# Optimization experiments

Hardware: AMD Instinct MI355X
Metric: run time of the kernel (lower is better)

The kernel has to match this reference:

```python
import jax, jax.numpy as jnp
import numpy as np

EPS = 1e-8


def setup_inputs() -> dict:
    key = jax.random.key(0)
    k1, k2 = jax.random.split(key)
    a = jax.random.normal(k1, (1, 256, 128, 128), dtype=jnp.float32)
    b = jax.random.normal(k2, (1, 256, 128, 128), dtype=jnp.float32)
    return {"a": a, "b": b}


def reference(a, b):
    # a: [n, c, h, w] rendered feats; b: [n, c, h2, w2] style feats (n == 1)
    n, c, h, w = a.shape
    a_flat = a.reshape(n, c, -1)            # [n, c, hw]
    b_flat = b.reshape(n, c, -1)            # [n, c, h2w2]

    # argmin_cos_distance: channel-wise L2 normalize, cosine distance, argmin
    b_norm = jnp.sqrt((b_flat * b_flat).sum(1, keepdims=True) + EPS)
    b_n = b_flat / (b_norm + EPS)
    a_norm = jnp.sqrt((a_flat * a_flat).sum(1, keepdims=True) + EPS)
    a_n = a_flat / (a_norm + EPS)
    d_mat = 1.0 - jnp.einsum('ncp,ncq->npq', a_n, b_n)   # [n, hw, h2w2]
    z_best = jnp.argmin(d_mat, axis=2)                    # [n, hw]

    # nn_feat_replace: gather matched (unnormalized) style features
    idx = jnp.broadcast_to(z_best[:, None, :], b_flat.shape)
    target = jnp.take_along_axis(b_flat, idx, axis=2).reshape(n, c, h, w)

    # cos_loss(a, target): cosine distance over channel dim, mean over pixels
    an = jnp.sqrt((a * a).sum(1, keepdims=True))
    tn = jnp.sqrt((target * target).sum(1, keepdims=True))
    cossim = ((a / (an + EPS)) * (target / (tn + EPS))).sum(1)  # [n, h, w]
    return (1.0 - cossim).mean()
```

## Files before the change

kernel.cpp:

```cpp
#include <hip/hip_runtime.h>
#include <stdint.h>

#define EPS 1e-8f

constexpr int HW = 16384;
constexpr int BM = 128;
constexpr int NG = 2048;

typedef __attribute__((ext_vector_type(4))) float floatx4;
typedef __attribute__((ext_vector_type(4))) int   intx4;
typedef __attribute__((ext_vector_type(8))) int   intx8;
typedef unsigned char u8;
typedef unsigned int u32;
typedef unsigned long long u64;

typedef const __attribute__((address_space(1))) u32 gas_u32;
typedef __attribute__((address_space(3))) u32 las_u32;
__device__ inline void stage16(const void* g, void* l) {
    __builtin_amdgcn_global_load_lds((gas_u32*)g, (las_u32*)l, 16, 0, 0);
}

__device__ inline u32 pk4(float x0, float x1, float x2, float x3) {
    int t = __builtin_amdgcn_cvt_pk_fp8_f32(x0, x1, 0, false);
    t = __builtin_amdgcn_cvt_pk_fp8_f32(x2, x3, t, true);
    return (u32)t;
}

__device__ inline float getc(const float4& f, int j) {
    return (j == 0) ? f.x : (j == 1) ? f.y : (j == 2) ? f.z : f.w;
}

__global__ __launch_bounds__(512) void prep_kernel(const float* __restrict__ a,
                                                   const float* __restrict__ b,
                                                   float* __restrict__ sumsq_a,
                                                   float* __restrict__ sumsq_b,
                                                   u8* __restrict__ aF, u8* __restrict__ bF,
                                                   u64* __restrict__ packed,
                                                   float* __restrict__ out) {
    __shared__ float red[64][33];
    __shared__ float invb_sh[32];
    const int tid = threadIdx.x;
    const int pg = tid & 7, tc = tid >> 3;
    const int p0 = blockIdx.x * 32, pb = pg * 4;
    const int c0 = tc * 4;
    const u32 fb = (u32)((c0 >> 7) * 2048 + ((c0 >> 4) & 1) * 1024 + (c0 & 15));
    const u32 qr16 = (u32)(((c0 >> 5) & 3) * 16);

    if (blockIdx.x < 32) packed[(size_t)blockIdx.x * 512 + tid] = 0ull;
    if (blockIdx.x == 0 && tid == 0) *out = 0.f;

    float4 bv[4], av[4];
    #pragma unroll
    for (int i = 0; i < 4; ++i)
        bv[i] = *(const float4*)&b[(size_t)(c0 + i) * HW + p0 + pb];
    #pragma unroll
    for (int i = 0; i < 4; ++i)
        av[i] = *(const float4*)&a[(size_t)(c0 + i) * HW + p0 + pb];

    float s0 = 0.f, s1 = 0.f, s2 = 0.f, s3 = 0.f;
    #pragma unroll
    for (int i = 0; i < 4; ++i) {
        s0 += bv[i].x * bv[i].x; s1 += bv[i].y * bv[i].y;
        s2 += bv[i].z * bv[i].z; s3 += bv[i].w * bv[i].w;
    }
    red[tc][pb] = s0; red[tc][pb + 1] = s1; red[tc][pb + 2] = s2; red[tc][pb + 3] = s3;
    __syncthreads();
    if (tid < 32) {
        float B = 0.f;
        #pragma unroll
        for (int j = 0; j < 64; ++j) B += red[j][tid];
        sumsq_b[p0 + tid] = B;
        invb_sh[tid] = 1.0f / (sqrtf(B + EPS) + EPS);
    }
    __syncthreads();

    #pragma unroll
    for (int j = 0; j < 4; ++j) {
        const int p = p0 + pb + j;
        const float inv = invb_sh[pb + j];
        u32 wv = pk4(getc(bv[0], j) * inv, getc(bv[1], j) * inv,
                     getc(bv[2], j) * inv, getc(bv[3], j) * inv);
        *(u32*)(bF + ((size_t)(p >> 4) << 12) + fb + (qr16 + (u32)(p & 15)) * 16) = wv;
    }

    s0 = s1 = s2 = s3 = 0.f;
    #pragma unroll
    for (int i = 0; i < 4; ++i) {
        s0 += av[i].x * av[i].x; s1 += av[i].y * av[i].y;
        s2 += av[i].z * av[i].z; s3 += av[i].w * av[i].w;
    }
    red[tc][pb] = s0; red[tc][pb + 1] = s1; red[tc][pb + 2] = s2; red[tc][pb + 3] = s3;
    #pragma unroll
    for (int j = 0; j < 4; ++j) {
        const int p = p0 + pb + j;
        u32 wv = pk4(getc(av[0], j), getc(av[1], j), getc(av[2], j), getc(av[3], j));
        *(u32*)(aF + ((size_t)(p >> 4) << 12) + fb + (qr16 + (u32)(p & 15)) * 16) = wv;
    }
    __syncthreads();
    if (tid < 32) {
        float A = 0.f;
        #pragma unroll
        for (int j = 0; j < 64; ++j) A += red[j][tid];
        sumsq_a[p0 + tid] = A;
    }
}

__global__ __launch_bounds__(256, 3) void gemm_argmax(const u8* __restrict__ aF,
                                                      const u8* __restrict__ bF,
                                                      u64* __restrict__ packed) {
    __shared__ u8 sB[2][16384];
    const int tid = threadIdx.x;
    const int w = tid >> 6, lane = tid & 63;
    const int q4 = lane >> 4, r15 = lane & 15;
    const int wm = w >> 1, wn = w & 1;

    const u32 bid = blockIdx.x;
    const u32 ng = bid & 7;
    const u32 mt = bid >> 3;
    const int p0 = (int)mt * BM;

    const u8* gA = aF + (((size_t)(mt * 8 + wm * 4)) << 12) + (u32)lane * 16;
    intx8 Afr[4][2];
    #pragma unroll
    for (int mi = 0; mi < 4; ++mi)
        #pragma unroll
        for (int kb = 0; kb < 2; ++kb) {
            intx4 lo = *(const intx4*)(gA + (u32)(mi * 4096 + kb * 2048));
            intx4 hi = *(const intx4*)(gA + (u32)(mi * 4096 + kb * 2048 + 1024));
            Afr[mi][kb] = __builtin_shufflevector(lo, hi, 0, 1, 2, 3, 4, 5, 6, 7);
        }

    const u8* gQ = bF + ((size_t)ng << 19);
    const u32 so = (u32)w * 4096u + (u32)lane * 16u;

    #pragma unroll
    for (int i = 0; i < 4; ++i)
        stage16(gQ + so + (u32)(i * 1024), &sB[0][w * 4096 + i * 1024]);

    float bestv[4][4];
    u32   bestq[4][4];
    #pragma unroll
    for (int mi = 0; mi < 4; ++mi)
        #pragma unroll
        for (int r = 0; r < 4; ++r) { bestv[mi][r] = -3.4e38f; bestq[mi][r] = 0; }

    u32 q0 = ng * 2048 + wn * 32 + (u32)r15;
    const floatx4 C64 = {64.f, 64.f, 64.f, 64.f};
    const int SCL = 0x7F7F7F7F;

    __syncthreads();

    int x = 0;
    for (int qt = 0; qt < 32; ++qt) {
        if (qt < 31) {
            const u8* gs = gQ + (u32)(qt + 1) * 16384u + so;
            u8* ls = &sB[x ^ 1][w * 4096];
            #pragma unroll
            for (int i = 0; i < 4; ++i)
                stage16(gs + (u32)(i * 1024), ls + i * 1024);
        }

        const u8* Lb = &sB[x][(u32)(wn * 2) * 4096u + (u32)lane * 16u];
        floatx4 acc[4][2];
        intx8 B0, B1;

        { intx4 lo = *(const intx4*)(Lb);
          intx4 hi = *(const intx4*)(Lb + 1024);
          B0 = __builtin_shufflevector(lo, hi, 0, 1, 2, 3, 4, 5, 6, 7); }
        { intx4 lo = *(const intx4*)(Lb + 4096);
          intx4 hi = *(const intx4*)(Lb + 4096 + 1024);
          B1 = __builtin_shufflevector(lo, hi, 0, 1, 2, 3, 4, 5, 6, 7); }
        __builtin_amdgcn_s_setprio(1);
        #pragma unroll
        for (int mi = 0; mi < 4; ++mi)
            acc[mi][0] = __builtin_amdgcn_mfma_scale_f32_16x16x128_f8f6f4(
                Afr[mi][0], B0, C64, 0, 0, 0, SCL, 0, SCL);
        #pragma unroll
        for (int mi = 0; mi < 4; ++mi)
            acc[mi][1] = __builtin_amdgcn_mfma_scale_f32_16x16x128_f8f6f4(
                Afr[mi][0], B1, C64, 0, 0, 0, SCL, 0, SCL);
        __builtin_amdgcn_s_setprio(0);

        { intx4 lo = *(const intx4*)(Lb + 2048);
          intx4 hi = *(const intx4*)(Lb + 2048 + 1024);
          B0 = __builtin_shufflevector(lo, hi, 0, 1, 2, 3, 4, 5, 6, 7); }
        { intx4 lo = *(const intx4*)(Lb + 4096 + 2048);
          intx4 hi = *(const intx4*)(Lb + 4096 + 2048 + 1024);
          B1 = __builtin_shufflevector(lo, hi, 0, 1, 2, 3, 4, 5, 6, 7); }
        __builtin_amdgcn_s_setprio(1);
        #pragma unroll
        for (int mi = 0; mi < 4; ++mi)
            acc[mi][0] = __builtin_amdgcn_mfma_scale_f32_16x16x128_f8f6f4(
                Afr[mi][1], B0, acc[mi][0], 0, 0, 0, SCL, 0, SCL);
        #pragma unroll
        for (int mi = 0; mi < 4; ++mi)
            acc[mi][1] = __builtin_amdgcn_mfma_scale_f32_16x16x128_f8f6f4(
                Afr[mi][1], B1, acc[mi][1], 0, 0, 0, SCL, 0, SCL);
        __builtin_amdgcn_s_setprio(0);

        #pragma unroll
        for (int mi = 0; mi < 4; ++mi)
            #pragma unroll
            for (int r = 0; r < 4; ++r) {
                float v = acc[mi][0][r];
                bool gt = v > bestv[mi][r];
                bestv[mi][r] = gt ? v : bestv[mi][r];
                bestq[mi][r] = gt ? q0 : bestq[mi][r];
            }
        #pragma unroll
        for (int mi = 0; mi < 4; ++mi)
            #pragma unroll
            for (int r = 0; r < 4; ++r) {
                float v = acc[mi][1][r];
                bool gt = v > bestv[mi][r];
                bestv[mi][r] = gt ? v : bestv[mi][r];
                bestq[mi][r] = gt ? (q0 + 16u) : bestq[mi][r];
            }
        q0 += 64u;

        __syncthreads();
        x ^= 1;
    }

    #pragma unroll
    for (int mi = 0; mi < 4; ++mi)
        #pragma unroll
        for (int r = 0; r < 4; ++r) {
            u64 pk = ((u64)__float_as_uint(bestv[mi][r]) << 32)
                   | (u64)(0xFFFFFFFFu - bestq[mi][r]);
            #pragma unroll
            for (int d = 1; d < 16; d <<= 1) {
                u64 o = __shfl_xor((unsigned long long)pk, d);
                pk = o > pk ? o : pk;
            }
            if (r15 == 0)
                atomicMax(&packed[p0 + wm * 64 + mi * 16 + q4 * 4 + r], pk);
        }
}

__global__ void loss_kernel(const u64* __restrict__ packed,
                            const float* __restrict__ sumsq_a, const float* __restrict__ sumsq_b,
                            float* __restrict__ out) {
    int p = blockIdx.x * 256 + threadIdx.x;
    u64 pk = packed[p];
    float s = __uint_as_float((u32)(pk >> 32)) - 64.0f;
    u32 q = 0xFFFFFFFFu - (u32)(pk & 0xFFFFFFFFull);
    float A = sumsq_a[p], B = sumsq_b[q];
    float dot = s * (sqrtf(B + EPS) + EPS);
    float cossim = dot / ((sqrtf(A) + EPS) * (sqrtf(B) + EPS));
    float v = (1.0f - cossim) * (1.0f / (float)HW);
    #pragma unroll
    for (int d = 1; d < 64; d <<= 1) v += __shfl_xor(v, d);
    if ((threadIdx.x & 63) == 0) atomicAdd(out, v);
}

extern "C" void kernel_launch(void* const* d_in, const int* in_sizes, int n_in,
                              void* d_out, int out_size, void* d_ws, size_t ws_size,
                              hipStream_t stream) {
    const float* a = (const float*)d_in[0];
    const float* b = (const float*)d_in[1];
    float* out = (float*)d_out;
    char* ws = (char*)d_ws;

    u8*    aF      = (u8*)ws;
    u8*    bF      = (u8*)(ws + (size_t)4 * 1024 * 1024);
    float* sumsq_a = (float*)(ws + (size_t)8 * 1024 * 1024);
    float* sumsq_b = sumsq_a + HW;
    u64*   packed  = (u64*)(sumsq_b + HW);

    prep_kernel<<<dim3(HW / 32), 512, 0, stream>>>(a, b, sumsq_a, sumsq_b, aF, bF, packed, out);
    gemm_argmax<<<dim3((HW / BM) * (HW / NG)), 256, 0, stream>>>(aF, bF, packed);
    loss_kernel<<<dim3(HW / 256), 256, 0, stream>>>(packed, sumsq_a, sumsq_b, out);
}
```

Before: 145.3 us.

## Double workgroup to 8 waves and software-pipeline MFMA with deferred argmax

```diff
diff --git a/kernel.cpp b/kernel.cpp
--- a/kernel.cpp
+++ b/kernel.cpp
@@ -105,7 +105,58 @@
     }
 }
 
-__global__ __launch_bounds__(256, 3) void gemm_argmax(const u8* __restrict__ aF,
+#define MFMA1(A_, B_, C_) __builtin_amdgcn_mfma_scale_f32_16x16x128_f8f6f4( \
+        (A_), (B_), (C_), 0, 0, 0, SCL, 0, SCL)
+
+#define LDB(off_) __builtin_shufflevector(                                  \
+        *(const intx4*)(Lb + (off_)), *(const intx4*)(Lb + (off_) + 1024),  \
+        0, 1, 2, 3, 4, 5, 6, 7)
+
+#define MFMA_QT(acc_, buf_) do {                                            \
+    const u8* Lb = &sB[buf_][(u32)(wn * 2) * 4096u + (u32)lane * 16u];      \
+    intx8 Bk0n0 = LDB(0);                                                   \
+    intx8 Bk0n1 = LDB(4096);                                                \
+    __builtin_amdgcn_s_setprio(1);                                          \
+    acc_[0][0] = MFMA1(Afr[0][0], Bk0n0, C64);                              \
+    acc_[1][0] = MFMA1(Afr[1][0], Bk0n0, C64);                              \
+    acc_[0][1] = MFMA1(Afr[0][0], Bk0n1, C64);                              \
+    acc_[1][1] = MFMA1(Afr[1][0], Bk0n1, C64);                              \
+    __builtin_amdgcn_s_setprio(0);                                          \
+    intx8 Bk1n0 = LDB(2048);                                                \
+    intx8 Bk1n1 = LDB(4096 + 2048);                                         \
+    __builtin_amdgcn_s_setprio(1);                                          \
+    acc_[0][0] = MFMA1(Afr[0][1], Bk1n0, acc_[0][0]);                       \
+    acc_[1][0] = MFMA1(Afr[1][1], Bk1n0, acc_[1][0]);                       \
+    acc_[0][1] = MFMA1(Afr[0][1], Bk1n1, acc_[0][1]);                       \
+    acc_[1][1] = MFMA1(Afr[1][1], Bk1n1, acc_[1][1]);                       \
+    __builtin_amdgcn_s_setprio(0);                                          \
+} while (0)
+
+#define ARGMAX_QT(acc_, qt_) do {                                           \
+    const u32 qb_ = q0 + (u32)(qt_) * 64u;                                  \
+    _Pragma("unroll")                                                       \
+    for (int mi = 0; mi < 2; ++mi) {                                        \
+        _Pragma("unroll")                                                   \
+        for (int ni = 0; ni < 2; ++ni) {                                    \
+            const u32 qc_ = qb_ + (u32)(ni * 16);                           \
+            _Pragma("unroll")                                               \
+            for (int r = 0; r < 4; ++r) {                                   \
+                float v_ = acc_[mi][ni][r];                                 \
+                bool gt_ = v_ > bestv[mi][r];                               \
+                bestv[mi][r] = gt_ ? v_ : bestv[mi][r];                     \
+                bestq[mi][r] = gt_ ? qc_ : bestq[mi][r];                    \
+            }                                                               \
+        }                                                                   \
+    }                                                                       \
+} while (0)
+
+#define STAGE(buf_, qt_) do {                                               \
+    const u8* gs_ = gQ + (u32)(qt_) * 16384u + so;                          \
+    stage16(gs_, &sB[buf_][wso]);                                           \
+    stage16(gs_ + 1024, &sB[buf_][wso + 1024]);                             \
+} while (0)
+
+__global__ __launch_bounds__(512, 4) void gemm_argmax(const u8* __restrict__ aF,
                                                       const u8* __restrict__ bF,
                                                       u64* __restrict__ packed) {
     __shared__ u8 sB[2][16384];
@@ -119,111 +170,70 @@
     const u32 mt = bid >> 3;
     const int p0 = (int)mt * BM;
 
-    const u8* gA = aF + (((size_t)(mt * 8 + wm * 4)) << 12) + (u32)lane * 16;
-    intx8 Afr[4][2];
-    #pragma unroll
-    for (int mi = 0; mi < 4; ++mi)
-        #pragma unroll
-        for (int kb = 0; kb < 2; ++kb) {
-            intx4 lo = *(const intx4*)(gA + (u32)(mi * 4096 + kb * 2048));
-            intx4 hi = *(const intx4*)(gA + (u32)(mi * 4096 + kb * 2048 + 1024));
-            Afr[mi][kb] = __builtin_shufflevector(lo, hi, 0, 1, 2, 3, 4, 5, 6, 7);
-        }
+    const u8* gA = aF + (((size_t)(mt * 8 + wm * 2)) << 12) + (u32)lane * 16;
+    intx8 Afr[2][2];
+    #pragma unroll
+    for (int mi = 0; mi < 2; ++mi)
+        #pragma unroll
+        for (int kb = 0; kb < 2; ++kb)
+            Afr[mi][kb] = __builtin_shufflevector(
+                *(const intx4*)(gA + (u32)(mi * 4096 + kb * 2048)),
+                *(const intx4*)(gA + (u32)(mi * 4096 + kb * 2048 + 1024)),
+                0, 1, 2, 3, 4, 5, 6, 7);
 
     const u8* gQ = bF + ((size_t)ng << 19);
-    const u32 so = (u32)w * 4096u + (u32)lane * 16u;
-
-    #pragma unroll
-    for (int i = 0; i < 4; ++i)
-        stage16(gQ + so + (u32)(i * 1024), &sB[0][w * 4096 + i * 1024]);
-
-    float bestv[4][4];
-    u32   bestq[4][4];
-    #pragma unroll
-    for (int mi = 0; mi < 4; ++mi)
+    const u32 so  = (u32)w * 2048u + (u32)lane * 16u;
+    const u32 wso = (u32)w * 2048u;
+
+    float bestv[2][4];
+    u32   bestq[2][4];
+    #pragma unroll
+    for (int mi = 0; mi < 2; ++mi)
         #pragma unroll
         for (int r = 0; r < 4; ++r) { bestv[mi][r] = -3.4e38f; bestq[mi][r] = 0; }
 
-    u32 q0 = ng * 2048 + wn * 32 + (u32)r15;
+    const u32 q0 = ng * 2048 + wn * 32 + (u32)r15;
     const floatx4 C64 = {64.f, 64.f, 64.f, 64.f};
     const int SCL = 0x7F7F7F7F;
 
-    __syncthreads();
-
-    int x = 0;
-    for (int qt = 0; qt < 32; ++qt) {
-        if (qt < 31) {
-            const u8* gs = gQ + (u32)(qt + 1) * 16384u + so;
-            u8* ls = &sB[x ^ 1][w * 4096];
-            #pragma unroll
-            for (int i = 0; i < 4; ++i)
-                stage16(gs + (u32)(i * 1024), ls + i * 1024);
-        }
-
-        const u8* Lb = &sB[x][(u32)(wn * 2) * 4096u + (u32)lane * 16u];
-        floatx4 acc[4][2];
-        intx8 B0, B1;
-
-        { intx4 lo = *(const intx4*)(Lb);
-          intx4 hi = *(const intx4*)(Lb + 1024);
-          B0 = __builtin_shufflevector(lo, hi, 0, 1, 2, 3, 4, 5, 6, 7); }
-        { intx4 lo = *(const intx4*)(Lb + 4096);
-          intx4 hi = *(const intx4*)(Lb + 4096 + 1024);
-          B1 = __builtin_shufflevector(lo, hi, 0, 1, 2, 3, 4, 5, 6, 7); }
-        __builtin_amdgcn_s_setprio(1);
-        #pragma unroll
-        for (int mi = 0; mi < 4; ++mi)
-            acc[mi][0] = __builtin_amdgcn_mfma_scale_f32_16x16x128_f8f6f4(
-                Afr[mi][0], B0, C64, 0, 0, 0, SCL, 0, SCL);
-        #pragma unroll
-        for (int mi = 0; mi < 4; ++mi)
-            acc[mi][1] = __builtin_amdgcn_mfma_scale_f32_16x16x128_f8f6f4(
-                Afr[mi][0], B1, C64, 0, 0, 0, SCL, 0, SCL);
-        __builtin_amdgcn_s_setprio(0);
-
-        { intx4 lo = *(const intx4*)(Lb + 2048);
-          intx4 hi = *(const intx4*)(Lb + 2048 + 1024);
-          B0 = __builtin_shufflevector(lo, hi, 0, 1, 2, 3, 4, 5, 6, 7); }
-        { intx4 lo = *(const intx4*)(Lb + 4096 + 2048);
-          intx4 hi = *(const intx4*)(Lb + 4096 + 2048 + 1024);
-          B1 = __builtin_shufflevector(lo, hi, 0, 1, 2, 3, 4, 5, 6, 7); }
-        __builtin_amdgcn_s_setprio(1);
-        #pragma unroll
-        for (int mi = 0; mi < 4; ++mi)
-            acc[mi][0] = __builtin_amdgcn_mfma_scale_f32_16x16x128_f8f6f4(
-                Afr[mi][1], B0, acc[mi][0], 0, 0, 0, SCL, 0, SCL);
-        #pragma unroll
-        for (int mi = 0; mi < 4; ++mi)
-            acc[mi][1] = __builtin_amdgcn_mfma_scale_f32_16x16x128_f8f6f4(
-                Afr[mi][1], B1, acc[mi][1], 0, 0, 0, SCL, 0, SCL);
-        __builtin_amdgcn_s_setprio(0);
-
-        #pragma unroll
-        for (int mi = 0; mi < 4; ++mi)
-            #pragma unroll
-            for (int r = 0; r < 4; ++r) {
-                float v = acc[mi][0][r];
-                bool gt = v > bestv[mi][r];
-                bestv[mi][r] = gt ? v : bestv[mi][r];
-                bestq[mi][r] = gt ? q0 : bestq[mi][r];
-            }
-        #pragma unroll
-        for (int mi = 0; mi < 4; ++mi)
-            #pragma unroll
-            for (int r = 0; r < 4; ++r) {
-                float v = acc[mi][1][r];
-                bool gt = v > bestv[mi][r];
-                bestv[mi][r] = gt ? v : bestv[mi][r];
-                bestq[mi][r] = gt ? (q0 + 16u) : bestq[mi][r];
-            }
-        q0 += 64u;
-
+    floatx4 accA[2][2], accB[2][2];
+
+    STAGE(0, 0);
+    __syncthreads();
+
+    STAGE(1, 1);
+    MFMA_QT(accA, 0);
+    __syncthreads();
+
+    STAGE(0, 2);
+    MFMA_QT(accB, 1);
+    ARGMAX_QT(accA, 0);
+    __syncthreads();
+
+    for (int i = 1; i <= 14; ++i) {
+        const int qtA = 2 * i;
+        STAGE(1, qtA + 1);
+        MFMA_QT(accA, 0);
+        ARGMAX_QT(accB, qtA - 1);
         __syncthreads();
-        x ^= 1;
-    }
-
-    #pragma unroll
-    for (int mi = 0; mi < 4; ++mi)
+
+        STAGE(0, qtA + 2);
+        MFMA_QT(accB, 1);
+        ARGMAX_QT(accA, qtA);
+        __syncthreads();
+    }
+
+    STAGE(1, 31);
+    MFMA_QT(accA, 0);
+    ARGMAX_QT(accB, 29);
+    __syncthreads();
+
+    MFMA_QT(accB, 1);
+    ARGMAX_QT(accA, 30);
+    ARGMAX_QT(accB, 31);
+
+    #pragma unroll
+    for (int mi = 0; mi < 2; ++mi)
         #pragma unroll
         for (int r = 0; r < 4; ++r) {
             u64 pk = ((u64)__float_as_uint(bestv[mi][r]) << 32)
@@ -234,7 +244,7 @@
                 pk = o > pk ? o : pk;
             }
             if (r15 == 0)
-                atomicMax(&packed[p0 + wm * 64 + mi * 16 + q4 * 4 + r], pk);
+                atomicMax(&packed[p0 + wm * 32 + mi * 16 + q4 * 4 + r], pk);
         }
 }
 
@@ -269,6 +279,6 @@
     u64*   packed  = (u64*)(sumsq_b + HW);
 
     prep_kernel<<<dim3(HW / 32), 512, 0, stream>>>(a, b, sumsq_a, sumsq_b, aF, bF, packed, out);
-    gemm_argmax<<<dim3((HW / BM) * (HW / NG)), 256, 0, stream>>>(aF, bF, packed);
+    gemm_argmax<<<dim3((HW / BM) * (HW / NG)), 512, 0, stream>>>(aF, bF, packed);
     loss_kernel<<<dim3(HW / 256), 256, 0, stream>>>(packed, sumsq_a, sumsq_b, out);
 }
```

New measurement: 165.7 us. 14.0% more time.

## Split prep into partial sum-of-squares pass and normalize/pack pass

Applied to the files above, without the earlier changes.

```diff
diff --git a/kernel.cpp b/kernel.cpp
--- a/kernel.cpp
+++ b/kernel.cpp
@@ -30,24 +30,63 @@
     return (j == 0) ? f.x : (j == 1) ? f.y : (j == 2) ? f.z : f.w;
 }
 
-__global__ __launch_bounds__(512) void prep_kernel(const float* __restrict__ a,
-                                                   const float* __restrict__ b,
-                                                   float* __restrict__ sumsq_a,
-                                                   float* __restrict__ sumsq_b,
-                                                   u8* __restrict__ aF, u8* __restrict__ bF,
-                                                   u64* __restrict__ packed,
-                                                   float* __restrict__ out) {
-    __shared__ float red[64][33];
-    __shared__ float invb_sh[32];
+__global__ __launch_bounds__(256) void prep1_kernel(const float* __restrict__ a,
+                                                    const float* __restrict__ b,
+                                                    float* __restrict__ apart,
+                                                    float* __restrict__ bpart,
+                                                    u64* __restrict__ packed,
+                                                    float* __restrict__ out) {
     const int tid = threadIdx.x;
-    const int pg = tid & 7, tc = tid >> 3;
-    const int p0 = blockIdx.x * 32, pb = pg * 4;
+    const u32 bid = blockIdx.x;
+    const int pg = (int)(bid >> 4), cg = (int)(bid & 15);
+    const int p = pg * 256 + tid;
+    const int c0 = cg * 16;
+
+    if (bid < 64) packed[(size_t)bid * 256 + tid] = 0ull;
+    if (bid == 0 && tid == 0) *out = 0.f;
+
+    float sb = 0.f, sa = 0.f;
+    #pragma unroll
+    for (int i = 0; i < 16; ++i) {
+        float xb = b[(size_t)(c0 + i) * HW + p];
+        sb += xb * xb;
+    }
+    #pragma unroll
+    for (int i = 0; i < 16; ++i) {
+        float xa = a[(size_t)(c0 + i) * HW + p];
+        sa += xa * xa;
+    }
+    bpart[(size_t)cg * HW + p] = sb;
+    apart[(size_t)cg * HW + p] = sa;
+}
+
+__global__ __launch_bounds__(256) void prep2_kernel(const float* __restrict__ a,
+                                                    const float* __restrict__ b,
+                                                    const float* __restrict__ apart,
+                                                    const float* __restrict__ bpart,
+                                                    float* __restrict__ sumsq_a,
+                                                    float* __restrict__ sumsq_b,
+                                                    u8* __restrict__ aF, u8* __restrict__ bF) {
+    __shared__ float invb_sh[16];
+    const int tid = threadIdx.x;
+    const int pg = tid & 3, tc = tid >> 2;
+    const int p0 = blockIdx.x * 16, pb = pg * 4;
     const int c0 = tc * 4;
     const u32 fb = (u32)((c0 >> 7) * 2048 + ((c0 >> 4) & 1) * 1024 + (c0 & 15));
     const u32 qr16 = (u32)(((c0 >> 5) & 3) * 16);
 
-    if (blockIdx.x < 32) packed[(size_t)blockIdx.x * 512 + tid] = 0ull;
-    if (blockIdx.x == 0 && tid == 0) *out = 0.f;
+    if (tid < 16) {
+        const int p = p0 + tid;
+        float B = 0.f, A = 0.f;
+        #pragma unroll
+        for (int j = 0; j < 16; ++j) {
+            B += bpart[(size_t)j * HW + p];
+            A += apart[(size_t)j * HW + p];
+        }
+        sumsq_b[p] = B;
+        sumsq_a[p] = A;
+        invb_sh[tid] = 1.0f / (sqrtf(B + EPS) + EPS);
+    }
 
     float4 bv[4], av[4];
     #pragma unroll
@@ -56,22 +95,6 @@
     #pragma unroll
     for (int i = 0; i < 4; ++i)
         av[i] = *(const float4*)&a[(size_t)(c0 + i) * HW + p0 + pb];
-
-    float s0 = 0.f, s1 = 0.f, s2 = 0.f, s3 = 0.f;
-    #pragma unroll
-    for (int i = 0; i < 4; ++i) {
-        s0 += bv[i].x * bv[i].x; s1 += bv[i].y * bv[i].y;
-        s2 += bv[i].z * bv[i].z; s3 += bv[i].w * bv[i].w;
-    }
-    red[tc][pb] = s0; red[tc][pb + 1] = s1; red[tc][pb + 2] = s2; red[tc][pb + 3] = s3;
-    __syncthreads();
-    if (tid < 32) {
-        float B = 0.f;
-        #pragma unroll
-        for (int j = 0; j < 64; ++j) B += red[j][tid];
-        sumsq_b[p0 + tid] = B;
-        invb_sh[tid] = 1.0f / (sqrtf(B + EPS) + EPS);
-    }
     __syncthreads();
 
     #pragma unroll
@@ -82,26 +105,11 @@
                      getc(bv[2], j) * inv, getc(bv[3], j) * inv);
         *(u32*)(bF + ((size_t)(p >> 4) << 12) + fb + (qr16 + (u32)(p & 15)) * 16) = wv;
     }
-
-    s0 = s1 = s2 = s3 = 0.f;
-    #pragma unroll
-    for (int i = 0; i < 4; ++i) {
-        s0 += av[i].x * av[i].x; s1 += av[i].y * av[i].y;
-        s2 += av[i].z * av[i].z; s3 += av[i].w * av[i].w;
-    }
-    red[tc][pb] = s0; red[tc][pb + 1] = s1; red[tc][pb + 2] = s2; red[tc][pb + 3] = s3;
     #pragma unroll
     for (int j = 0; j < 4; ++j) {
         const int p = p0 + pb + j;
         u32 wv = pk4(getc(av[0], j), getc(av[1], j), getc(av[2], j), getc(av[3], j));
         *(u32*)(aF + ((size_t)(p >> 4) << 12) + fb + (qr16 + (u32)(p & 15)) * 16) = wv;
-    }
-    __syncthreads();
-    if (tid < 32) {
-        float A = 0.f;
-        #pragma unroll
-        for (int j = 0; j < 64; ++j) A += red[j][tid];
-        sumsq_a[p0 + tid] = A;
     }
 }
 
@@ -124,11 +132,11 @@
     #pragma unroll
     for (int mi = 0; mi < 4; ++mi)
         #pragma unroll
-        for (int kb = 0; kb < 2; ++kb) {
-            intx4 lo = *(const intx4*)(gA + (u32)(mi * 4096 + kb * 2048));
-            intx4 hi = *(const intx4*)(gA + (u32)(mi * 4096 + kb * 2048 + 1024));
-            Afr[mi][kb] = __builtin_shufflevector(lo, hi, 0, 1, 2, 3, 4, 5, 6, 7);
-        }
+        for (int kb = 0; kb < 2; ++kb)
+            Afr[mi][kb] = __builtin_shufflevector(
+                *(const intx4*)(gA + (u32)(mi * 4096 + kb * 2048)),
+                *(const intx4*)(gA + (u32)(mi * 4096 + kb * 2048 + 1024)),
+                0, 1, 2, 3, 4, 5, 6, 7);
 
     const u8* gQ = bF + ((size_t)ng << 19);
     const u32 so = (u32)w * 4096u + (u32)lane * 16u;
@@ -267,8 +275,12 @@
     float* sumsq_a = (float*)(ws + (size_t)8 * 1024 * 1024);
     float* sumsq_b = sumsq_a + HW;
     u64*   packed  = (u64*)(sumsq_b + HW);
-
-    prep_kernel<<<dim3(HW / 32), 512, 0, stream>>>(a, b, sumsq_a, sumsq_b, aF, bF, packed, out);
+    float* apart   = (float*)(ws + (size_t)8 * 1024 * 1024 + 256 * 1024);
+    float* bpart   = apart + 16 * HW;
+
+    prep1_kernel<<<dim3(1024), 256, 0, stream>>>(a, b, apart, bpart, packed, out);
+    prep2_kernel<<<dim3(HW / 16), 256, 0, stream>>>(a, b, apart, bpart,
+                                                    sumsq_a, sumsq_b, aF, bF);
     gemm_argmax<<<dim3((HW / BM) * (HW / NG)), 256, 0, stream>>>(aF, bF, packed);
     loss_kernel<<<dim3(HW / 256), 256, 0, stream>>>(packed, sumsq_a, sumsq_b, out);
 }
```

New measurement: 154.7 us. 1.06x slower.

## Move b normalization from prep into GEMM epilogue, simplify prep kernel

Applied to the files above, without the earlier changes.

```diff
diff --git a/kernel.cpp b/kernel.cpp
--- a/kernel.cpp
+++ b/kernel.cpp
@@ -26,89 +26,59 @@
     return (u32)t;
 }
 
-__device__ inline float getc(const float4& f, int j) {
-    return (j == 0) ? f.x : (j == 1) ? f.y : (j == 2) ? f.z : f.w;
-}
-
-__global__ __launch_bounds__(512) void prep_kernel(const float* __restrict__ a,
+__global__ __launch_bounds__(256) void prep_kernel(const float* __restrict__ a,
                                                    const float* __restrict__ b,
                                                    float* __restrict__ sumsq_a,
                                                    float* __restrict__ sumsq_b,
                                                    u8* __restrict__ aF, u8* __restrict__ bF,
                                                    u64* __restrict__ packed,
                                                    float* __restrict__ out) {
-    __shared__ float red[64][33];
-    __shared__ float invb_sh[32];
+    __shared__ float redb[8][33];
+    __shared__ float reda[8][33];
     const int tid = threadIdx.x;
-    const int pg = tid & 7, tc = tid >> 3;
-    const int p0 = blockIdx.x * 32, pb = pg * 4;
-    const int c0 = tc * 4;
-    const u32 fb = (u32)((c0 >> 7) * 2048 + ((c0 >> 4) & 1) * 1024 + (c0 & 15));
-    const u32 qr16 = (u32)(((c0 >> 5) & 3) * 16);
-
-    if (blockIdx.x < 32) packed[(size_t)blockIdx.x * 512 + tid] = 0ull;
+    const int px = tid & 31, wg = tid >> 5;
+    const int p0 = blockIdx.x * 32;
+    const int p = p0 + px;
+    const int c0 = wg * 32;
+
+    if (blockIdx.x < 64) packed[(size_t)blockIdx.x * 256 + tid] = 0ull;
     if (blockIdx.x == 0 && tid == 0) *out = 0.f;
 
-    float4 bv[4], av[4];
-    #pragma unroll
-    for (int i = 0; i < 4; ++i)
-        bv[i] = *(const float4*)&b[(size_t)(c0 + i) * HW + p0 + pb];
-    #pragma unroll
-    for (int i = 0; i < 4; ++i)
-        av[i] = *(const float4*)&a[(size_t)(c0 + i) * HW + p0 + pb];
-
-    float s0 = 0.f, s1 = 0.f, s2 = 0.f, s3 = 0.f;
-    #pragma unroll
-    for (int i = 0; i < 4; ++i) {
-        s0 += bv[i].x * bv[i].x; s1 += bv[i].y * bv[i].y;
-        s2 += bv[i].z * bv[i].z; s3 += bv[i].w * bv[i].w;
-    }
-    red[tc][pb] = s0; red[tc][pb + 1] = s1; red[tc][pb + 2] = s2; red[tc][pb + 3] = s3;
+    const u32 slab = ((u32)(p >> 4)) << 12;
+    const u32 r16 = (u32)(p & 15) * 16;
+
+    float sb = 0.f, sa = 0.f;
+    #pragma unroll
+    for (int k = 0; k < 8; ++k) {
+        const int c = c0 + k * 4;
+        const u32 fo = (u32)((c >> 7) * 2048 + ((c >> 4) & 1) * 1024 + (c & 15))
+                     + (u32)(((c >> 5) & 3) * 256) + r16;
+        float x0 = b[(size_t)(c + 0) * HW + p], x1 = b[(size_t)(c + 1) * HW + p];
+        float x2 = b[(size_t)(c + 2) * HW + p], x3 = b[(size_t)(c + 3) * HW + p];
+        sb += x0 * x0 + x1 * x1 + x2 * x2 + x3 * x3;
+        *(u32*)(bF + slab + fo) = pk4(x0, x1, x2, x3);
+        float y0 = a[(size_t)(c + 0) * HW + p], y1 = a[(size_t)(c + 1) * HW + p];
+        float y2 = a[(size_t)(c + 2) * HW + p], y3 = a[(size_t)(c + 3) * HW + p];
+        sa += y0 * y0 + y1 * y1 + y2 * y2 + y3 * y3;
+        *(u32*)(aF + slab + fo) = pk4(y0, y1, y2, y3);
+    }
+    redb[wg][px] = sb; reda[wg][px] = sa;
     __syncthreads();
     if (tid < 32) {
-        float B = 0.f;
-        #pragma unroll
-        for (int j = 0; j < 64; ++j) B += red[j][tid];
+        float B = 0.f, A = 0.f;
+        #pragma unroll
+        for (int j = 0; j < 8; ++j) { B += redb[j][tid]; A += reda[j][tid]; }
         sumsq_b[p0 + tid] = B;
-        invb_sh[tid] = 1.0f / (sqrtf(B + EPS) + EPS);
-    }
-    __syncthreads();
-
-    #pragma unroll
-    for (int j = 0; j < 4; ++j) {
-        const int p = p0 + pb + j;
-        const float inv = invb_sh[pb + j];
-        u32 wv = pk4(getc(bv[0], j) * inv, getc(bv[1], j) * inv,
-                     getc(bv[2], j) * inv, getc(bv[3], j) * inv);
-        *(u32*)(bF + ((size_t)(p >> 4) << 12) + fb + (qr16 + (u32)(p & 15)) * 16) = wv;
-    }
-
-    s0 = s1 = s2 = s3 = 0.f;
-    #pragma unroll
-    for (int i = 0; i < 4; ++i) {
-        s0 += av[i].x * av[i].x; s1 += av[i].y * av[i].y;
-        s2 += av[i].z * av[i].z; s3 += av[i].w * av[i].w;
-    }
-    red[tc][pb] = s0; red[tc][pb + 1] = s1; red[tc][pb + 2] = s2; red[tc][pb + 3] = s3;
-    #pragma unroll
-    for (int j = 0; j < 4; ++j) {
-        const int p = p0 + pb + j;
-        u32 wv = pk4(getc(av[0], j), getc(av[1], j), getc(av[2], j), getc(av[3], j));
-        *(u32*)(aF + ((size_t)(p >> 4) << 12) + fb + (qr16 + (u32)(p & 15)) * 16) = wv;
-    }
-    __syncthreads();
-    if (tid < 32) {
-        float A = 0.f;
-        #pragma unroll
-        for (int j = 0; j < 64; ++j) A += red[j][tid];
         sumsq_a[p0 + tid] = A;
     }
 }
 
 __global__ __launch_bounds__(256, 3) void gemm_argmax(const u8* __restrict__ aF,
                                                       const u8* __restrict__ bF,
+                                                      const float* __restrict__ sumsq_b,
                                                       u64* __restrict__ packed) {
     __shared__ u8 sB[2][16384];
+    __shared__ float invb_lds[2048];
     const int tid = threadIdx.x;
     const int w = tid >> 6, lane = tid & 63;
     const int q4 = lane >> 4, r15 = lane & 15;
@@ -124,11 +94,18 @@
     #pragma unroll
     for (int mi = 0; mi < 4; ++mi)
         #pragma unroll
-        for (int kb = 0; kb < 2; ++kb) {
-            intx4 lo = *(const intx4*)(gA + (u32)(mi * 4096 + kb * 2048));
-            intx4 hi = *(const intx4*)(gA + (u32)(mi * 4096 + kb * 2048 + 1024));
-            Afr[mi][kb] = __builtin_shufflevector(lo, hi, 0, 1, 2, 3, 4, 5, 6, 7);
-        }
+        for (int kb = 0; kb < 2; ++kb)
+            Afr[mi][kb] = __builtin_shufflevector(
+                *(const intx4*)(gA + (u32)(mi * 4096 + kb * 2048)),
+                *(const intx4*)(gA + (u32)(mi * 4096 + kb * 2048 + 1024)),
+                0, 1, 2, 3, 4, 5, 6, 7);
+
+    #pragma unroll
+    for (int i = 0; i < 8; ++i) {
+        int idx = tid + i * 256;
+        float B = sumsq_b[ng * 2048 + idx];
+        invb_lds[idx] = 1.0f / (sqrtf(B + EPS) + EPS);
+    }
 
     const u8* gQ = bF + ((size_t)ng << 19);
     const u32 so = (u32)w * 4096u + (u32)lane * 16u;
@@ -145,7 +122,7 @@
         for (int r = 0; r < 4; ++r) { bestv[mi][r] = -3.4e38f; bestq[mi][r] = 0; }
 
     u32 q0 = ng * 2048 + wn * 32 + (u32)r15;
-    const floatx4 C64 = {64.f, 64.f, 64.f, 64.f};
+    const floatx4 Z = {0.f, 0.f, 0.f, 0.f};
     const int SCL = 0x7F7F7F7F;
 
     __syncthreads();
@@ -174,11 +151,11 @@
         #pragma unroll
         for (int mi = 0; mi < 4; ++mi)
             acc[mi][0] = __builtin_amdgcn_mfma_scale_f32_16x16x128_f8f6f4(
-                Afr[mi][0], B0, C64, 0, 0, 0, SCL, 0, SCL);
+                Afr[mi][0], B0, Z, 0, 0, 0, SCL, 0, SCL);
         #pragma unroll
         for (int mi = 0; mi < 4; ++mi)
             acc[mi][1] = __builtin_amdgcn_mfma_scale_f32_16x16x128_f8f6f4(
-                Afr[mi][0], B1, C64, 0, 0, 0, SCL, 0, SCL);
+                Afr[mi][0], B1, Z, 0, 0, 0, SCL, 0, SCL);
         __builtin_amdgcn_s_setprio(0);
 
         { intx4 lo = *(const intx4*)(Lb + 2048);
@@ -198,11 +175,14 @@
                 Afr[mi][1], B1, acc[mi][1], 0, 0, 0, SCL, 0, SCL);
         __builtin_amdgcn_s_setprio(0);
 
+        const u32 pc = (u32)qt * 64u + (u32)(wn * 32) + (u32)r15;
+        const float inv0 = invb_lds[pc];
+        const float inv1 = invb_lds[pc + 16];
         #pragma unroll
         for (int mi = 0; mi < 4; ++mi)
             #pragma unroll
             for (int r = 0; r < 4; ++r) {
-                float v = acc[mi][0][r];
+                float v = acc[mi][0][r] * inv0;
                 bool gt = v > bestv[mi][r];
                 bestv[mi][r] = gt ? v : bestv[mi][r];
                 bestq[mi][r] = gt ? q0 : bestq[mi][r];
@@ -211,7 +191,7 @@
         for (int mi = 0; mi < 4; ++mi)
             #pragma unroll
             for (int r = 0; r < 4; ++r) {
-                float v = acc[mi][1][r];
+                float v = acc[mi][1][r] * inv1;
                 bool gt = v > bestv[mi][r];
                 bestv[mi][r] = gt ? v : bestv[mi][r];
                 bestq[mi][r] = gt ? (q0 + 16u) : bestq[mi][r];
@@ -226,8 +206,9 @@
     for (int mi = 0; mi < 4; ++mi)
         #pragma unroll
         for (int r = 0; r < 4; ++r) {
-            u64 pk = ((u64)__float_as_uint(bestv[mi][r]) << 32)
-                   | (u64)(0xFFFFFFFFu - bestq[mi][r]);
+            u32 m = __float_as_uint(bestv[mi][r]);
+            m = m ^ (u32)(((int)m >> 31) | 0x80000000u);
+            u64 pk = ((u64)m << 32) | (u64)(0xFFFFFFFFu - bestq[mi][r]);
             #pragma unroll
             for (int d = 1; d < 16; d <<= 1) {
                 u64 o = __shfl_xor((unsigned long long)pk, d);
@@ -243,7 +224,9 @@
                             float* __restrict__ out) {
     int p = blockIdx.x * 256 + threadIdx.x;
     u64 pk = packed[p];
-    float s = __uint_as_float((u32)(pk >> 32)) - 64.0f;
+    u32 m = (u32)(pk >> 32);
+    u32 u = (m & 0x80000000u) ? (m ^ 0x80000000u) : ~m;
+    float s = __uint_as_float(u);
     u32 q = 0xFFFFFFFFu - (u32)(pk & 0xFFFFFFFFull);
     float A = sumsq_a[p], B = sumsq_b[q];
     float dot = s * (sqrtf(B + EPS) + EPS);
@@ -268,7 +251,7 @@
     float* sumsq_b = sumsq_a + HW;
     u64*   packed  = (u64*)(sumsq_b + HW);
 
-    prep_kernel<<<dim3(HW / 32), 512, 0, stream>>>(a, b, sumsq_a, sumsq_b, aF, bF, packed, out);
-    gemm_argmax<<<dim3((HW / BM) * (HW / NG)), 256, 0, stream>>>(aF, bF, packed);
+    prep_kernel<<<dim3(HW / 32), 256, 0, stream>>>(a, b, sumsq_a, sumsq_b, aF, bF, packed, out);
+    gemm_argmax<<<dim3((HW / BM) * (HW / NG)), 256, 0, stream>>>(aF, bF, sumsq_b, packed);
     loss_kernel<<<dim3(HW / 256), 256, 0, stream>>>(packed, sumsq_a, sumsq_b, out);
 }
```

Result: slower. 179.3 us (+23.4%).
